# Kernel optimization log

Hardware: AMD Instinct MI355X
Metric: run time of the kernel (lower is better)

## Reference

```python
import jax, jax.numpy as jnp
import numpy as np

N_EMBD = 1024
HEAD_SIZE = 64
T = 8192
LN_EPS = 1e-5


def _layer_norm(x, gamma, beta):
    mu = jnp.mean(x, axis=-1, keepdims=True)
    var = jnp.mean(jnp.square(x - mu), axis=-1, keepdims=True)
    return (x - mu) * jax.lax.rsqrt(var + LN_EPS) * gamma + beta


def setup_inputs() -> dict:
    key = jax.random.key(0)
    ks = jax.random.split(key, 10)
    s_in = 1.0 / np.sqrt(N_EMBD)
    s_hs = 1.0 / np.sqrt(HEAD_SIZE)
    s_ff = 1.0 / np.sqrt(4 * N_EMBD)
    return {
        "x": jax.random.normal(ks[0], (T, N_EMBD), dtype=jnp.float32),
        "Wk": jax.random.uniform(ks[1], (N_EMBD, HEAD_SIZE), jnp.float32, -s_in, s_in),
        "Wq": jax.random.uniform(ks[2], (N_EMBD, HEAD_SIZE), jnp.float32, -s_in, s_in),
        "Wv": jax.random.uniform(ks[3], (N_EMBD, HEAD_SIZE), jnp.float32, -s_in, s_in),
        "Wp": jax.random.uniform(ks[4], (HEAD_SIZE, N_EMBD), jnp.float32, -s_hs, s_hs),
        "W1": jax.random.uniform(ks[5], (N_EMBD, 4 * N_EMBD), jnp.float32, -s_in, s_in),
        "b1": jax.random.uniform(ks[6], (4 * N_EMBD,), jnp.float32, -s_in, s_in),
        "W2": jax.random.uniform(ks[7], (4 * N_EMBD, N_EMBD), jnp.float32, -s_ff, s_ff),
        "b2": jax.random.uniform(ks[8], (N_EMBD,), jnp.float32, -s_ff, s_ff),
        "g1": jnp.ones((N_EMBD,), jnp.float32),
        "be1": jnp.zeros((N_EMBD,), jnp.float32),
        "g2": jnp.ones((N_EMBD,), jnp.float32),
        "be2": jnp.zeros((N_EMBD,), jnp.float32),
    }


def reference(x, Wk, Wq, Wv, Wp, W1, b1, W2, b2, g1, be1, g2, be2):
    Tn = x.shape[0]
    k = x @ Wk            # (T, hs)
    q = x @ Wq            # (T, hs)
    v = x @ Wv            # (T, hs)
    wei = (q @ k.T) * (HEAD_SIZE ** -0.5)       # (T, T)
    causal = jnp.tril(jnp.ones((Tn, Tn), dtype=bool))
    wei = jnp.where(causal, wei, -jnp.inf)
    wei = jax.nn.softmax(wei, axis=-1)
    attn = (wei @ v) @ Wp                        # (T, n_embd)
    x1 = _layer_norm(x + attn, g1, be1)
    y = jax.nn.relu(x1 @ W1 + b1) @ W2 + b2      # FFN
    return _layer_norm(x1 + y, g2, be2)
```

## Files before the change

kernel.cpp:

```cpp
#include <hip/hip_runtime.h>
#include <hip/hip_bf16.h>

#define T_SEQ 8192
#define NE 1024
#define FF 4096

typedef __bf16 bf16_t;
typedef __bf16 bf16x8 __attribute__((ext_vector_type(8)));
typedef __bf16 bf16x4 __attribute__((ext_vector_type(4)));
typedef float f32x4 __attribute__((ext_vector_type(4)));

__device__ __forceinline__ void gll16(const void* g, void* l) {
    __builtin_amdgcn_global_load_lds(
        (const __attribute__((address_space(1))) void*)g,
        (__attribute__((address_space(3))) void*)l, 16, 0, 0);
}

__global__ __launch_bounds__(256) void cast_f32_bf16(const float* __restrict__ in,
                                                     bf16_t* __restrict__ out, int n4) {
    int i = blockIdx.x * 256 + threadIdx.x;
    if (i >= n4) return;
    float4 v = ((const float4*)in)[i];
    bf16x4 h;
    h[0] = (bf16_t)v.x; h[1] = (bf16_t)v.y; h[2] = (bf16_t)v.z; h[3] = (bf16_t)v.w;
    ((bf16x4*)out)[i] = h;
}

__global__ __launch_bounds__(256) void build_wkqv(const float* __restrict__ Wk,
                                                  const float* __restrict__ Wq,
                                                  const float* __restrict__ Wv,
                                                  bf16_t* __restrict__ out) {
    int idx = blockIdx.x * 256 + threadIdx.x;
    int n  = idx >> 10;
    int kk = idx & 1023;
    float v = 0.f;
    if (n < 64)       v = Wk[kk * 64 + n];
    else if (n < 128) v = Wq[kk * 64 + (n - 64)] * 0.125f;
    else if (n < 192) v = Wv[kk * 64 + (n - 128)];
    out[idx] = (bf16_t)v;
}

__global__ __launch_bounds__(256) void tcast(const float* __restrict__ in,
                                             bf16_t* __restrict__ out, int R, int C) {
    __shared__ bf16_t tl[64][66];
    const int bc = blockIdx.x << 6, br = blockIdx.y << 6;
    const int tx = threadIdx.x & 63, ty = threadIdx.x >> 6;
#pragma unroll
    for (int j = 0; j < 16; ++j) {
        const int r = ty + j * 4;
        tl[r][tx] = (bf16_t)in[(size_t)(br + r) * C + bc + tx];
    }
    __syncthreads();
#pragma unroll
    for (int j = 0; j < 16; ++j) {
        const int r = ty + j * 4;
        out[(size_t)(bc + r) * R + br + tx] = tl[tx][r];
    }
}

template <int EPI>
__global__ __launch_bounds__(256, 2)
void gemm_bt(const bf16_t* __restrict__ A, const bf16_t* __restrict__ Bt,
             int M, int N, int K,
             float* __restrict__ outf,
             bf16_t* __restrict__ ob0, bf16_t* __restrict__ ob1, bf16_t* __restrict__ ob2,
             const float* __restrict__ res, const float* __restrict__ bias) {
    const int tid  = threadIdx.x;
    const int lane = tid & 63;
    const int tiles_n = N >> 7;
    const int tm = blockIdx.x / tiles_n;
    const int tn = blockIdx.x % tiles_n;
    const int brow = tm << 7, bcol = tn << 7;

    __shared__ __align__(16) bf16_t As[128 * 32];
    __shared__ __align__(16) bf16_t Bs[128 * 32];

    const int c1 = tid, c2 = tid + 256;
    const int s1 = (((c1 & 3) ^ ((c1 >> 3) & 3)) * 8);
    const int s2 = (((c2 & 3) ^ ((c2 >> 3) & 3)) * 8);
    const bf16_t* gA1 = A + (size_t)(brow + (c1 >> 2)) * K + s1;
    const bf16_t* gA2 = A + (size_t)(brow + (c2 >> 2)) * K + s2;
    const bf16_t* gB1 = Bt + (size_t)(bcol + (c1 >> 2)) * K + s1;
    const bf16_t* gB2 = Bt + (size_t)(bcol + (c2 >> 2)) * K + s2;
    bf16_t* lA1 = As + c1 * 8; bf16_t* lA2 = As + c2 * 8;
    bf16_t* lB1 = Bs + c1 * 8; bf16_t* lB2 = Bs + c2 * 8;

    const int wv = tid >> 6;
    const int wr = (wv >> 1) * 64, wc = (wv & 1) * 64;
    const int arow  = wr + (lane & 15);
    const int brf   = wc + (lane & 15);
    const int koff = (((lane >> 4) ^ ((lane >> 1) & 3)) * 8);

    f32x4 acc[4][4];
#pragma unroll
    for (int i = 0; i < 4; ++i)
#pragma unroll
        for (int j = 0; j < 4; ++j) acc[i][j] = (f32x4){0.f, 0.f, 0.f, 0.f};

    for (int k0 = 0; k0 < K; k0 += 32) {
        gll16(gA1, lA1); gll16(gA2, lA2);
        gll16(gB1, lB1); gll16(gB2, lB2);
        gA1 += 32; gA2 += 32; gB1 += 32; gB2 += 32;
        __syncthreads();
        bf16x8 af[4], bfr[4];
#pragma unroll
        for (int mi = 0; mi < 4; ++mi)
            af[mi] = *(const bf16x8*)(As + (arow + mi * 16) * 32 + koff);
#pragma unroll
        for (int ni = 0; ni < 4; ++ni)
            bfr[ni] = *(const bf16x8*)(Bs + (brf + ni * 16) * 32 + koff);
#pragma unroll
        for (int mi = 0; mi < 4; ++mi)
#pragma unroll
            for (int ni = 0; ni < 4; ++ni)
                acc[mi][ni] = __builtin_amdgcn_mfma_f32_16x16x32_bf16(
                    af[mi], bfr[ni], acc[mi][ni], 0, 0, 0);
        __syncthreads();
    }

    const int r0 = brow + wr + ((lane >> 4) << 2);
    const int c0 = bcol + wc + (lane & 15);
#pragma unroll
    for (int mi = 0; mi < 4; ++mi)
#pragma unroll
        for (int ni = 0; ni < 4; ++ni)
#pragma unroll
            for (int r = 0; r < 4; ++r) {
                const int row = r0 + mi * 16 + r;
                const int col = c0 + ni * 16;
                const float v = acc[mi][ni][r];
                if constexpr (EPI == 0) {
                    if (col < 64)       ob0[row * 64 + col] = (bf16_t)v;
                    else if (col < 128) ob1[row * 64 + (col - 64)] = (bf16_t)v;
                    else if (col < 192) ob2[(size_t)(col - 128) * T_SEQ + row] = (bf16_t)v;
                } else if constexpr (EPI == 1) {
                    outf[(size_t)row * N + col] = res[(size_t)row * N + col] + v;
                } else if constexpr (EPI == 2) {
                    ob0[(size_t)row * N + col] = (bf16_t)fmaxf(v + bias[col], 0.f);
                } else {
                    outf[(size_t)row * N + col] = res[(size_t)row * N + col] + v + bias[col];
                }
            }
}

template <int EPI>
__global__ __launch_bounds__(512, 1)
void gemm_ls(const bf16_t* __restrict__ A, int lda,
             const bf16_t* __restrict__ Bt, int ldb,
             int N, int K,
             bf16_t* __restrict__ ob, const float* __restrict__ bias,
             float* __restrict__ po0, float* __restrict__ po1) {
    __shared__ __align__(16) bf16_t sA[4][8192];
    __shared__ __align__(16) bf16_t sB[4][8192];
    const int tid = threadIdx.x, lane = tid & 63, w = tid >> 6;
    const int wm = w >> 2, wn = w & 3;

    const int nwg = gridDim.x;
    const int wgid = (blockIdx.x & 7) * (nwg >> 3) + (blockIdx.x >> 3);
    const int tiles_n = N >> 8;
    const int tm = wgid / tiles_n, tn = wgid % tiles_n;
    const int brow = tm << 8, bcol = tn << 8;
    const size_t kofs = (size_t)blockIdx.y * K;

    const int s0 = (w & 1) * 2, rbb = w >> 1;
    const bf16_t* gA0 = A + (size_t)(brow + rbb * 64 + lane) * lda + kofs + s0 * 8;
    const bf16_t* gB0 = Bt + (size_t)(bcol + rbb * 64 + lane) * ldb + kofs + s0 * 8;
    const int dA0 = s0 * 2048 + (rbb * 64 + lane) * 8;

    const int l15 = lane & 15, sq = lane >> 4;
    const int aoff = sq * 2048 + (wm * 128 + l15) * 8;
    const int boff = sq * 2048 + (wn * 64 + l15) * 8;
    const int NTS = K >> 5;

    f32x4 acc[8][4];
#pragma unroll
    for (int i = 0; i < 8; ++i)
#pragma unroll
        for (int j = 0; j < 4; ++j) acc[i][j] = (f32x4){0.f, 0.f, 0.f, 0.f};
    bf16x8 af[8], bfr[4];

#define L_SB  __builtin_amdgcn_sched_barrier(0)
#define L_BAR { L_SB; __builtin_amdgcn_s_barrier(); L_SB; }
#define L_LG0 { asm volatile("s_waitcnt lgkmcnt(0)" ::: "memory"); L_SB; }
#define L_VM4 { asm volatile("s_waitcnt vmcnt(4)" ::: "memory"); L_SB; }
#define L_VM0 { asm volatile("s_waitcnt vmcnt(0)" ::: "memory"); L_SB; }
#define L_STAGE(t) { const int q_ = (t) & 3; \
    gll16(gA0 + (size_t)(t) * 32,        &sA[q_][dA0]); \
    gll16(gA0 + (size_t)(t) * 32 + 8,    &sA[q_][dA0 + 2048]); \
    gll16(gB0 + (size_t)(t) * 32,        &sB[q_][dA0]); \
    gll16(gB0 + (size_t)(t) * 32 + 8,    &sB[q_][dA0 + 2048]); \
    L_SB; }
#define L_DS(t) { const int q_ = (t) & 3; \
    _Pragma("unroll") for (int m = 0; m < 8; ++m) \
        af[m] = *(const bf16x8*)(&sA[q_][aoff + m * 128]); \
    _Pragma("unroll") for (int n = 0; n < 4; ++n) \
        bfr[n] = *(const bf16x8*)(&sB[q_][boff + n * 128]); }
#define L_MMA() { __builtin_amdgcn_s_setprio(1); \
    _Pragma("unroll") for (int m = 0; m < 8; ++m) \
    _Pragma("unroll") for (int n = 0; n < 4; ++n) \
        acc[m][n] = __builtin_amdgcn_mfma_f32_16x16x32_bf16(af[m], bfr[n], acc[m][n], 0, 0, 0); \
    __builtin_amdgcn_s_setprio(0); }

    L_STAGE(0); L_STAGE(1);
    L_VM4; L_BAR;
    for (int t = 0; t < NTS - 2; ++t) {
        L_DS(t);
        L_STAGE(t + 2);
        L_LG0;
        L_MMA();
        L_VM4; L_BAR;
    }
    L_DS(NTS - 2); L_LG0; L_MMA(); L_VM0; L_BAR;
    L_DS(NTS - 1); L_LG0; L_MMA();

#undef L_MMA
#undef L_DS
#undef L_STAGE
#undef L_VM0
#undef L_VM4
#undef L_LG0
#undef L_BAR
#undef L_SB

    const int r0 = brow + wm * 128 + sq * 4;
    const int c0 = bcol + wn * 64 + l15;
    float* po = blockIdx.y ? po1 : po0;
#pragma unroll
    for (int m = 0; m < 8; ++m)
#pragma unroll
        for (int n = 0; n < 4; ++n) {
            const int col = c0 + n * 16;
#pragma unroll
            for (int r = 0; r < 4; ++r) {
                const int row = r0 + m * 16 + r;
                const float v = acc[m][n][r];
                if constexpr (EPI == 2) {
                    ob[(size_t)row * N + col] = (bf16_t)fmaxf(v + bias[col], 0.f);
                } else {
                    po[(size_t)row * N + col] = v;
                }
            }
        }
}

__global__ __launch_bounds__(256)
void attn_partial(const bf16_t* __restrict__ Q, const bf16_t* __restrict__ Kb,
                  const bf16_t* __restrict__ VT,
                  float* __restrict__ po, float* __restrict__ pml) {
    const int tid = threadIdx.x, lane = tid & 63, w = tid >> 6;
    const int j = blockIdx.x * 4 + w;

    int a = 0;
    while (j >= 16 * (a + 1) * (a + 2)) ++a;
    const int r_in = j - 16 * a * (a + 1);
    const int idx = r_in / (a + 1);
    const int chunk = r_in - idx * (a + 1);
    const int g = a * 8 + (idx >> 2);
    const int qi = g * 4 + (idx & 3);

    __shared__ __align__(16) bf16_t P[4][16 * 64];
    const int l15 = lane & 15, hi = lane >> 4;
    const int koff = hi * 8;
    const int qrow = qi * 16 + l15;
    const bf16x8 qf0 = *(const bf16x8*)(Q + qrow * 64 + koff);
    const bf16x8 qf1 = *(const bf16x8*)(Q + qrow * 64 + 32 + koff);

    float m_run[4], l_run[4];
    f32x4 oacc[4];
#pragma unroll
    for (int r = 0; r < 4; ++r) { m_run[r] = -1e30f; l_run[r] = 0.f; }
#pragma unroll
    for (int d = 0; d < 4; ++d) oacc[d] = (f32x4){0.f, 0.f, 0.f, 0.f};

    const int t0 = chunk * 8;
    const int t1 = min(t0 + 8, g + 1);
    for (int t = t0; t < t1; ++t) {
        const int kv0 = t << 6;
        f32x4 s[4];
#pragma unroll
        for (int ni = 0; ni < 4; ++ni) s[ni] = (f32x4){0.f, 0.f, 0.f, 0.f};
#pragma unroll
        for (int ni = 0; ni < 4; ++ni) {
            const bf16_t* kp = Kb + (kv0 + ni * 16 + l15) * 64 + koff;
            bf16x8 kf0 = *(const bf16x8*)(kp);
            bf16x8 kf1 = *(const bf16x8*)(kp + 32);
            s[ni] = __builtin_amdgcn_mfma_f32_16x16x32_bf16(qf0, kf0, s[ni], 0, 0, 0);
            s[ni] = __builtin_amdgcn_mfma_f32_16x16x32_bf16(qf1, kf1, s[ni], 0, 0, 0);
        }
        if (t == g) {
#pragma unroll
            for (int ni = 0; ni < 4; ++ni)
#pragma unroll
                for (int r = 0; r < 4; ++r) {
                    const int col = kv0 + ni * 16 + l15;
                    const int row = qi * 16 + hi * 4 + r;
                    if (col > row) s[ni][r] = -1e30f;
                }
        }
        float pv[4][4], alpha[4];
#pragma unroll
        for (int r = 0; r < 4; ++r) {
            float vm = fmaxf(fmaxf(s[0][r], s[1][r]), fmaxf(s[2][r], s[3][r]));
            vm = fmaxf(vm, __shfl_xor(vm, 1));
            vm = fmaxf(vm, __shfl_xor(vm, 2));
            vm = fmaxf(vm, __shfl_xor(vm, 4));
            vm = fmaxf(vm, __shfl_xor(vm, 8));
            const float mnew = fmaxf(m_run[r], vm);
            float sum = 0.f;
#pragma unroll
            for (int ni = 0; ni < 4; ++ni) {
                float p = __expf(s[ni][r] - mnew);
                pv[ni][r] = p; sum += p;
            }
            sum += __shfl_xor(sum, 1); sum += __shfl_xor(sum, 2);
            sum += __shfl_xor(sum, 4); sum += __shfl_xor(sum, 8);
            alpha[r] = __expf(m_run[r] - mnew);
            l_run[r] = l_run[r] * alpha[r] + sum;
            m_run[r] = mnew;
        }
#pragma unroll
        for (int d = 0; d < 4; ++d)
#pragma unroll
            for (int r = 0; r < 4; ++r) oacc[d][r] *= alpha[r];
        asm volatile("s_waitcnt lgkmcnt(0)" ::: "memory");
        __builtin_amdgcn_sched_barrier(0);
#pragma unroll
        for (int ni = 0; ni < 4; ++ni)
#pragma unroll
            for (int r = 0; r < 4; ++r)
                P[w][(hi * 4 + r) * 64 + ni * 16 + l15] = (bf16_t)pv[ni][r];
        asm volatile("s_waitcnt lgkmcnt(0)" ::: "memory");
        __builtin_amdgcn_sched_barrier(0);
#pragma unroll
        for (int ks = 0; ks < 2; ++ks) {
            bf16x8 pf = *(const bf16x8*)(&P[w][l15 * 64 + ks * 32 + koff]);
#pragma unroll
            for (int d = 0; d < 4; ++d) {
                bf16x8 vf = *(const bf16x8*)(VT + (size_t)(d * 16 + l15) * T_SEQ + kv0 + ks * 32 + koff);
                oacc[d] = __builtin_amdgcn_mfma_f32_16x16x32_bf16(pf, vf, oacc[d], 0, 0, 0);
            }
        }
    }
#pragma unroll
    for (int d = 0; d < 4; ++d)
#pragma unroll
        for (int r = 0; r < 4; ++r)
            po[(size_t)j * 1024 + (hi * 4 + r) * 64 + d * 16 + l15] = oacc[d][r];
    if (l15 == 0) {
#pragma unroll
        for (int r = 0; r < 4; ++r) {
            pml[(size_t)j * 32 + hi * 4 + r] = m_run[r];
            pml[(size_t)j * 32 + 16 + hi * 4 + r] = l_run[r];
        }
    }
}

__global__ __launch_bounds__(256)
void attn_reduce(const float* __restrict__ po, const float* __restrict__ pml,
                 bf16_t* __restrict__ O) {
    const int qi = blockIdx.x;
    const int tid = threadIdx.x;
    const int row = tid >> 4;
    const int cg = tid & 15;
    const int g = qi >> 2;
    const int a = g >> 3;
    const int idx = ((g & 7) << 2) | (qi & 3);
    const int base = 16 * a * (a + 1) + idx * (a + 1);
    const int cnt = a + 1;

    float M = -1e30f;
    for (int i = 0; i < cnt; ++i)
        M = fmaxf(M, pml[(size_t)(base + i) * 32 + row]);
    float L = 0.f;
    f32x4 o = (f32x4){0.f, 0.f, 0.f, 0.f};
    for (int i = 0; i < cnt; ++i) {
        const float m = pml[(size_t)(base + i) * 32 + row];
        const float l = pml[(size_t)(base + i) * 32 + 16 + row];
        const float wgt = __expf(m - M);
        L += l * wgt;
        const f32x4 v = *(const f32x4*)&po[(size_t)(base + i) * 1024 + row * 64 + cg * 4];
#pragma unroll
        for (int u = 0; u < 4; ++u) o[u] += v[u] * wgt;
    }
    const float inv = 1.f / L;
    bf16x4 h;
#pragma unroll
    for (int u = 0; u < 4; ++u) h[u] = (bf16_t)(o[u] * inv);
    *(bf16x4*)(O + (size_t)(qi * 16 + row) * 64 + cg * 4) = h;
}

__global__ __launch_bounds__(256)
void ln_fused(const float* __restrict__ in, const float* __restrict__ g,
              const float* __restrict__ b, float* __restrict__ o32,
              bf16_t* __restrict__ o16) {
    const int row = blockIdx.x, tid = threadIdx.x;
    const float4 v = ((const float4*)(in + (size_t)row * NE))[tid];
    float s = v.x + v.y + v.z + v.w;
    float ss = v.x * v.x + v.y * v.y + v.z * v.z + v.w * v.w;
#pragma unroll
    for (int off = 1; off < 64; off <<= 1) {
        s  += __shfl_xor(s, off);
        ss += __shfl_xor(ss, off);
    }
    __shared__ float red[8];
    const int wv = tid >> 6, lane = tid & 63;
    if (lane == 0) { red[wv] = s; red[4 + wv] = ss; }
    __syncthreads();
    s  = red[0] + red[1] + red[2] + red[3];
    ss = red[4] + red[5] + red[6] + red[7];
    const float mu = s * (1.f / NE);
    const float rstd = rsqrtf(ss * (1.f / NE) - mu * mu + 1e-5f);
    const float4 gg = ((const float4*)g)[tid];
    const float4 bb = ((const float4*)b)[tid];
    float4 o;
    o.x = (v.x - mu) * rstd * gg.x + bb.x;
    o.y = (v.y - mu) * rstd * gg.y + bb.y;
    o.z = (v.z - mu) * rstd * gg.z + bb.z;
    o.w = (v.w - mu) * rstd * gg.w + bb.w;
    if (o32) ((float4*)(o32 + (size_t)row * NE))[tid] = o;
    if (o16) {
        bf16x4 h;
        h[0] = (bf16_t)o.x; h[1] = (bf16_t)o.y; h[2] = (bf16_t)o.z; h[3] = (bf16_t)o.w;
        *(bf16x4*)(o16 + (size_t)row * NE + tid * 4) = h;
    }
}

__global__ __launch_bounds__(256)
void ln_sum(const float* __restrict__ r1, const float* __restrict__ p0,
            const float* __restrict__ p1, const float* __restrict__ bias,
            const float* __restrict__ g, const float* __restrict__ b,
            float* __restrict__ out) {
    const int row = blockIdx.x, tid = threadIdx.x;
    const size_t off = (size_t)row * NE;
    const float4 a = ((const float4*)(r1 + off))[tid];
    const float4 q0 = ((const float4*)(p0 + off))[tid];
    const float4 q1 = ((const float4*)(p1 + off))[tid];
    const float4 bb4 = ((const float4*)bias)[tid];
    float4 v;
    v.x = a.x + q0.x + q1.x + bb4.x;
    v.y = a.y + q0.y + q1.y + bb4.y;
    v.z = a.z + q0.z + q1.z + bb4.z;
    v.w = a.w + q0.w + q1.w + bb4.w;
    float s = v.x + v.y + v.z + v.w;
    float ss = v.x * v.x + v.y * v.y + v.z * v.z + v.w * v.w;
#pragma unroll
    for (int off2 = 1; off2 < 64; off2 <<= 1) {
        s  += __shfl_xor(s, off2);
        ss += __shfl_xor(ss, off2);
    }
    __shared__ float red[8];
    const int wv = tid >> 6, lane = tid & 63;
    if (lane == 0) { red[wv] = s; red[4 + wv] = ss; }
    __syncthreads();
    s  = red[0] + red[1] + red[2] + red[3];
    ss = red[4] + red[5] + red[6] + red[7];
    const float mu = s * (1.f / NE);
    const float rstd = rsqrtf(ss * (1.f / NE) - mu * mu + 1e-5f);
    const float4 gg = ((const float4*)g)[tid];
    const float4 be = ((const float4*)b)[tid];
    float4 o;
    o.x = (v.x - mu) * rstd * gg.x + be.x;
    o.y = (v.y - mu) * rstd * gg.y + be.y;
    o.z = (v.z - mu) * rstd * gg.z + be.z;
    o.w = (v.w - mu) * rstd * gg.w + be.w;
    ((float4*)(out + off))[tid] = o;
}

extern "C" void kernel_launch(void* const* d_in, const int* in_sizes, int n_in,
                              void* d_out, int out_size, void* d_ws, size_t ws_size,
                              hipStream_t stream) {
    (void)in_sizes; (void)n_in; (void)out_size; (void)ws_size;
    const float* x   = (const float*)d_in[0];
    const float* Wk  = (const float*)d_in[1];
    const float* Wq  = (const float*)d_in[2];
    const float* Wv  = (const float*)d_in[3];
    const float* Wp  = (const float*)d_in[4];
    const float* W1  = (const float*)d_in[5];
    const float* b1  = (const float*)d_in[6];
    const float* W2  = (const float*)d_in[7];
    const float* b2  = (const float*)d_in[8];
    const float* g1  = (const float*)d_in[9];
    const float* be1 = (const float*)d_in[10];
    const float* g2  = (const float*)d_in[11];
    const float* be2 = (const float*)d_in[12];
    float* out = (float*)d_out;

    char* ws = (char*)d_ws;
    bf16_t* xb   = (bf16_t*)(ws);
    bf16_t* x1b  = (bf16_t*)(ws + 16777216);
    bf16_t* hb   = (bf16_t*)(ws + 33554432);
    float*  po   = (float*)(ws + 33554432);
    float*  pml  = (float*)(ws + 33554432 + 18874368);
    bf16_t* W1t  = (bf16_t*)(ws + 100663296);
    bf16_t* W2t  = (bf16_t*)(ws + 109051904);
    bf16_t* Wkqv = (bf16_t*)(ws + 117440512);
    bf16_t* WpT  = (bf16_t*)(ws + 117964800);
    bf16_t* kb   = (bf16_t*)(ws + 118095872);
    bf16_t* qb   = (bf16_t*)(ws + 119144448);
    bf16_t* vT   = (bf16_t*)(ws + 120193024);
    bf16_t* a0   = (bf16_t*)(ws + 121241600);
    float*  r1   = (float*)(ws + 122290176);
    float*  pk0  = (float*)(ws + 155844608);
    float*  pk1  = (float*)(ws);

    cast_f32_bf16<<<8192, 256, 0, stream>>>(x, xb, 2097152);
    build_wkqv<<<1024, 256, 0, stream>>>(Wk, Wq, Wv, Wkqv);
    tcast<<<dim3(16, 1), 256, 0, stream>>>(Wp, WpT, 64, 1024);
    tcast<<<dim3(64, 16), 256, 0, stream>>>(W1, W1t, 1024, 4096);
    tcast<<<dim3(16, 64), 256, 0, stream>>>(W2, W2t, 4096, 1024);

    gemm_bt<0><<<64 * 2, 256, 0, stream>>>(xb, Wkqv, 8192, 256, 1024,
                                           nullptr, kb, qb, vT, nullptr, nullptr);
    attn_partial<<<1088, 256, 0, stream>>>(qb, kb, vT, po, pml);
    attn_reduce<<<512, 256, 0, stream>>>(po, pml, a0);
    gemm_bt<1><<<64 * 8, 256, 0, stream>>>(a0, WpT, 8192, 1024, 64,
                                           r1, nullptr, nullptr, nullptr, x, nullptr);
    ln_fused<<<8192, 256, 0, stream>>>(r1, g1, be1, r1, x1b);
    gemm_ls<2><<<dim3(512, 1), 512, 0, stream>>>(x1b, 1024, W1t, 1024, 4096, 1024,
                                                 hb, b1, nullptr, nullptr);
    gemm_ls<4><<<dim3(128, 2), 512, 0, stream>>>(hb, 4096, W2t, 4096, 1024, 2048,
                                                 nullptr, nullptr, pk0, pk1);
    ln_sum<<<8192, 256, 0, stream>>>(r1, pk0, pk1, b2, g2, be2, out);
}
```

Baseline: 355.3 us.

## Double-buffer register fragments and deepen LDS prefetch in GEMM mainloop

The GEMM mainloop now keeps two sets of A/B register fragments, so the LDS reads for the next k-step are issued before the MFMAs of the current step, and waits use a partial lgkmcnt. Global-to-LDS staging runs three stages ahead instead of two, with barriers placed around the stage writes. The goal is to hide LDS read latency and global load latency behind MFMA work. In exchange, the doubled fragment registers may lower occupancy or cause spills, and the extra barrier per iteration adds sync cost.

```diff
diff --git a/kernel.cpp b/kernel.cpp
--- a/kernel.cpp
+++ b/kernel.cpp
@@ -177,11 +177,12 @@
     for (int i = 0; i < 8; ++i)
 #pragma unroll
         for (int j = 0; j < 4; ++j) acc[i][j] = (f32x4){0.f, 0.f, 0.f, 0.f};
-    bf16x8 af[8], bfr[4];
+    bf16x8 afA[8], bfA[4], afB[8], bfB[4];
 
 #define L_SB  __builtin_amdgcn_sched_barrier(0)
 #define L_BAR { L_SB; __builtin_amdgcn_s_barrier(); L_SB; }
-#define L_LG0 { asm volatile("s_waitcnt lgkmcnt(0)" ::: "memory"); L_SB; }
+#define L_LGK12 { asm volatile("s_waitcnt lgkmcnt(12)" ::: "memory"); L_SB; }
+#define L_LGK0  { asm volatile("s_waitcnt lgkmcnt(0)" ::: "memory"); L_SB; }
 #define L_VM4 { asm volatile("s_waitcnt vmcnt(4)" ::: "memory"); L_SB; }
 #define L_VM0 { asm volatile("s_waitcnt vmcnt(0)" ::: "memory"); L_SB; }
 #define L_STAGE(t) { const int q_ = (t) & 3; \
@@ -190,35 +191,52 @@
     gll16(gB0 + (size_t)(t) * 32,        &sB[q_][dA0]); \
     gll16(gB0 + (size_t)(t) * 32 + 8,    &sB[q_][dA0 + 2048]); \
     L_SB; }
-#define L_DS(t) { const int q_ = (t) & 3; \
+#define L_DS(t, AF, BF) { const int q_ = (t) & 3; \
     _Pragma("unroll") for (int m = 0; m < 8; ++m) \
-        af[m] = *(const bf16x8*)(&sA[q_][aoff + m * 128]); \
+        AF[m] = *(const bf16x8*)(&sA[q_][aoff + m * 128]); \
     _Pragma("unroll") for (int n = 0; n < 4; ++n) \
-        bfr[n] = *(const bf16x8*)(&sB[q_][boff + n * 128]); }
-#define L_MMA() { __builtin_amdgcn_s_setprio(1); \
+        BF[n] = *(const bf16x8*)(&sB[q_][boff + n * 128]); }
+#define L_MMA(AF, BF) { __builtin_amdgcn_s_setprio(1); \
     _Pragma("unroll") for (int m = 0; m < 8; ++m) \
     _Pragma("unroll") for (int n = 0; n < 4; ++n) \
-        acc[m][n] = __builtin_amdgcn_mfma_f32_16x16x32_bf16(af[m], bfr[n], acc[m][n], 0, 0, 0); \
+        acc[m][n] = __builtin_amdgcn_mfma_f32_16x16x32_bf16(AF[m], BF[n], acc[m][n], 0, 0, 0); \
     __builtin_amdgcn_s_setprio(0); }
-
-    L_STAGE(0); L_STAGE(1);
+#define L_BODY(t, CA, CB, NA, NB) { \
+    L_DS((t) + 1, NA, NB); \
+    L_LGK12; \
+    L_MMA(CA, CB); \
+    L_BAR; \
+    L_STAGE((t) + 3); \
+    L_VM4; \
+    L_BAR; }
+
+    L_STAGE(0); L_STAGE(1); L_STAGE(2);
     L_VM4; L_BAR;
-    for (int t = 0; t < NTS - 2; ++t) {
-        L_DS(t);
-        L_STAGE(t + 2);
-        L_LG0;
-        L_MMA();
-        L_VM4; L_BAR;
-    }
-    L_DS(NTS - 2); L_LG0; L_MMA(); L_VM0; L_BAR;
-    L_DS(NTS - 1); L_LG0; L_MMA();
-
+    L_DS(0, afA, bfA);
+
+    for (int t = 0; t < NTS - 4; t += 2) {
+        L_BODY(t,     afA, bfA, afB, bfB);
+        L_BODY(t + 1, afB, bfB, afA, bfA);
+    }
+    L_BODY(NTS - 4, afA, bfA, afB, bfB);
+    L_DS(NTS - 2, afA, bfA);
+    L_LGK12;
+    L_MMA(afB, bfB);
+    L_BAR; L_VM0; L_BAR;
+    L_DS(NTS - 1, afB, bfB);
+    L_LGK12;
+    L_MMA(afA, bfA);
+    L_LGK0;
+    L_MMA(afB, bfB);
+
+#undef L_BODY
 #undef L_MMA
 #undef L_DS
 #undef L_STAGE
 #undef L_VM0
 #undef L_VM4
-#undef L_LG0
+#undef L_LGK0
+#undef L_LGK12
 #undef L_BAR
 #undef L_SB
 
```

Result: slower. 393.1 us (+10.6%).

## Split GEMM main loop into two half-tile phases with interleaved loads

Applied to the files above, without the earlier changes.

Restructures the bf16 GEMM K-loop so each 32-wide K step runs as two phases of 16 MFMAs over half the A fragments, interleaving LDS reads and global-to-LDS staging of A and B between them. This halves the A fragment registers, which could allow better register allocation or occupancy, and spreads memory issue across the step in a ping-pong style. In exchange it adds extra workgroup barriers per iteration, which may serialize waves and hurt overlap.

```diff
diff --git a/kernel.cpp b/kernel.cpp
--- a/kernel.cpp
+++ b/kernel.cpp
@@ -177,48 +177,63 @@
     for (int i = 0; i < 8; ++i)
 #pragma unroll
         for (int j = 0; j < 4; ++j) acc[i][j] = (f32x4){0.f, 0.f, 0.f, 0.f};
-    bf16x8 af[8], bfr[4];
+    bf16x8 af[4], bfr[4];
 
 #define L_SB  __builtin_amdgcn_sched_barrier(0)
 #define L_BAR { L_SB; __builtin_amdgcn_s_barrier(); L_SB; }
-#define L_LG0 { asm volatile("s_waitcnt lgkmcnt(0)" ::: "memory"); L_SB; }
+#define L_LGK0 { asm volatile("s_waitcnt lgkmcnt(0)" ::: "memory"); L_SB; }
 #define L_VM4 { asm volatile("s_waitcnt vmcnt(4)" ::: "memory"); L_SB; }
 #define L_VM0 { asm volatile("s_waitcnt vmcnt(0)" ::: "memory"); L_SB; }
-#define L_STAGE(t) { const int q_ = (t) & 3; \
-    gll16(gA0 + (size_t)(t) * 32,        &sA[q_][dA0]); \
-    gll16(gA0 + (size_t)(t) * 32 + 8,    &sA[q_][dA0 + 2048]); \
-    gll16(gB0 + (size_t)(t) * 32,        &sB[q_][dA0]); \
-    gll16(gB0 + (size_t)(t) * 32 + 8,    &sB[q_][dA0 + 2048]); \
-    L_SB; }
-#define L_DS(t) { const int q_ = (t) & 3; \
-    _Pragma("unroll") for (int m = 0; m < 8; ++m) \
-        af[m] = *(const bf16x8*)(&sA[q_][aoff + m * 128]); \
+#define L_STAGE_A(t) { const int q_ = (t) & 3; \
+    gll16(gA0 + (size_t)(t) * 32,     &sA[q_][dA0]); \
+    gll16(gA0 + (size_t)(t) * 32 + 8, &sA[q_][dA0 + 2048]); }
+#define L_STAGE_B(t) { const int q_ = (t) & 3; \
+    gll16(gB0 + (size_t)(t) * 32,     &sB[q_][dA0]); \
+    gll16(gB0 + (size_t)(t) * 32 + 8, &sB[q_][dA0 + 2048]); }
+#define L_DS_A(t, mb) { const int q_ = (t) & 3; \
+    _Pragma("unroll") for (int m = 0; m < 4; ++m) \
+        af[m] = *(const bf16x8*)(&sA[q_][aoff + ((mb) + m) * 128]); }
+#define L_DS_B(t) { const int q_ = (t) & 3; \
     _Pragma("unroll") for (int n = 0; n < 4; ++n) \
         bfr[n] = *(const bf16x8*)(&sB[q_][boff + n * 128]); }
-#define L_MMA() { __builtin_amdgcn_s_setprio(1); \
-    _Pragma("unroll") for (int m = 0; m < 8; ++m) \
+#define L_MMA(mb) { __builtin_amdgcn_s_setprio(1); \
+    _Pragma("unroll") for (int m = 0; m < 4; ++m) \
     _Pragma("unroll") for (int n = 0; n < 4; ++n) \
-        acc[m][n] = __builtin_amdgcn_mfma_f32_16x16x32_bf16(af[m], bfr[n], acc[m][n], 0, 0, 0); \
+        acc[(mb) + m][n] = __builtin_amdgcn_mfma_f32_16x16x32_bf16(af[m], bfr[n], acc[(mb) + m][n], 0, 0, 0); \
     __builtin_amdgcn_s_setprio(0); }
-
-    L_STAGE(0); L_STAGE(1);
+#define L_BODY(t) { \
+    L_DS_A(t, 0); L_DS_B(t); L_STAGE_A((t) + 2); L_SB; \
+    L_BAR; L_LGK0; L_MMA(0); L_BAR; \
+    L_DS_A(t, 4); L_STAGE_B((t) + 2); L_SB; \
+    L_BAR; L_LGK0; L_MMA(4); \
+    L_VM4; L_BAR; }
+
+    L_STAGE_A(0); L_STAGE_B(0);
+    L_STAGE_A(1); L_STAGE_B(1);
     L_VM4; L_BAR;
-    for (int t = 0; t < NTS - 2; ++t) {
-        L_DS(t);
-        L_STAGE(t + 2);
-        L_LG0;
-        L_MMA();
-        L_VM4; L_BAR;
-    }
-    L_DS(NTS - 2); L_LG0; L_MMA(); L_VM0; L_BAR;
-    L_DS(NTS - 1); L_LG0; L_MMA();
-
+
+    for (int t = 0; t < NTS - 2; ++t)
+        L_BODY(t);
+
+    L_DS_A(NTS - 2, 0); L_DS_B(NTS - 2);
+    L_BAR; L_LGK0; L_MMA(0); L_BAR;
+    L_DS_A(NTS - 2, 4);
+    L_BAR; L_LGK0; L_MMA(4);
+    L_VM0; L_BAR;
+    L_DS_A(NTS - 1, 0); L_DS_B(NTS - 1);
+    L_LGK0; L_MMA(0);
+    L_DS_A(NTS - 1, 4);
+    L_LGK0; L_MMA(4);
+
+#undef L_BODY
 #undef L_MMA
-#undef L_DS
-#undef L_STAGE
+#undef L_DS_B
+#undef L_DS_A
+#undef L_STAGE_B
+#undef L_STAGE_A
 #undef L_VM0
 #undef L_VM4
-#undef L_LG0
+#undef L_LGK0
 #undef L_BAR
 #undef L_SB
 
```

Measured after the change: 413.1 us. 16.3% more time.
